# Performance work log

Measured on AMD Instinct MI355X. Metric: run time of the kernel, lower is better.

Reference implementation:

```python
import jax, jax.numpy as jnp
import numpy as np

B = 2; C = 3; IMG = 224; P = 16
DIM = 256; DEPTH = 2; HEADS = 4; DH = 64; MLP = 1024; NCLS = 1000
GRID = IMG // P            # 14
NPATCH = GRID * GRID       # 196
T = NPATCH + 1             # 197 (cls token)
PATCH_DIM = C * P * P      # 768


def _ln(x, g, b):
    m = x.mean(-1, keepdims=True)
    v = ((x - m) ** 2).mean(-1, keepdims=True)
    return (x - m) * jax.lax.rsqrt(v + 1e-5) * g + b


def _trittention(x, ln_g, ln_b, w_abcde, b_abcde, w_out, b_out):
    b, t, _ = x.shape
    xn = _ln(x, ln_g, ln_b)
    abcde = xn @ w_abcde + b_abcde                      # [b,t,5*H*DH]
    a, bb, c, d, e = jnp.split(abcde, 5, axis=-1)
    rs = lambda z: z.reshape(b, t, HEADS, DH)
    a, bb, c, d, e = map(rs, (a, bb, c, d, e))
    # cubic ternary scores: [b, h, q, s, t]
    s = jnp.einsum('bshd,bthd,bqhd->bhqst', a, bb, c) / DH
    p = jax.nn.softmax(s.reshape(b, HEADS, t, t * t), axis=-1)
    p = p.reshape(b, HEADS, t, t, t)
    z = jnp.einsum('bhqlr,blhd->bhqd', p, d) + jnp.einsum('bhqlr,brhd->bhqd', p, e)
    z = z.transpose(0, 2, 1, 3).reshape(b, t, HEADS * DH)
    return z @ w_out + b_out


def _ff(x, ln_g, ln_b, w1, b1, w2, b2):
    h = jax.nn.gelu(_ln(x, ln_g, ln_b) @ w1 + b1, approximate=False)
    return h @ w2 + b2


def setup_inputs() -> dict:
    key = jax.random.key(0)
    ks = jax.random.split(key, 10)
    s = 0.02
    d = {}
    d['img'] = jax.random.normal(ks[0], (B, C, IMG, IMG), jnp.float32)
    d['patch_ln1_g'] = jnp.ones((PATCH_DIM,), jnp.float32)
    d['patch_ln1_b'] = jnp.zeros((PATCH_DIM,), jnp.float32)
    d['patch_w'] = jax.random.normal(ks[1], (PATCH_DIM, DIM), jnp.float32) * s
    d['patch_b'] = jnp.zeros((DIM,), jnp.float32)
    d['patch_ln2_g'] = jnp.ones((DIM,), jnp.float32)
    d['patch_ln2_b'] = jnp.zeros((DIM,), jnp.float32)
    d['pos_emb'] = jax.random.normal(ks[2], (1, T, DIM), jnp.float32) * s
    d['cls_token'] = jax.random.normal(ks[3], (1, 1, DIM), jnp.float32) * s
    d['attn_ln_g'] = jnp.ones((DEPTH, DIM), jnp.float32)
    d['attn_ln_b'] = jnp.zeros((DEPTH, DIM), jnp.float32)
    d['w_abcde'] = jax.random.normal(ks[4], (DEPTH, DIM, 5 * HEADS * DH), jnp.float32) * s
    d['b_abcde'] = jnp.zeros((DEPTH, 5 * HEADS * DH), jnp.float32)
    d['w_out'] = jax.random.normal(ks[5], (DEPTH, HEADS * DH, DIM), jnp.float32) * s
    d['b_out'] = jnp.zeros((DEPTH, DIM), jnp.float32)
    d['ff_ln_g'] = jnp.ones((DEPTH, DIM), jnp.float32)
    d['ff_ln_b'] = jnp.zeros((DEPTH, DIM), jnp.float32)
    d['ff_w1'] = jax.random.normal(ks[6], (DEPTH, DIM, MLP), jnp.float32) * s
    d['ff_b1'] = jnp.zeros((DEPTH, MLP), jnp.float32)
    d['ff_w2'] = jax.random.normal(ks[7], (DEPTH, MLP, DIM), jnp.float32) * s
    d['ff_b2'] = jnp.zeros((DEPTH, DIM), jnp.float32)
    d['final_ln_g'] = jnp.ones((DIM,), jnp.float32)
    d['final_ln_b'] = jnp.zeros((DIM,), jnp.float32)
    d['head_w'] = jax.random.normal(ks[8], (DIM, NCLS), jnp.float32) * s
    d['head_b'] = jnp.zeros((NCLS,), jnp.float32)
    return d


def reference(img, patch_ln1_g, patch_ln1_b, patch_w, patch_b, patch_ln2_g, patch_ln2_b,
              pos_emb, cls_token, attn_ln_g, attn_ln_b, w_abcde, b_abcde, w_out, b_out,
              ff_ln_g, ff_ln_b, ff_w1, ff_b1, ff_w2, ff_b2, final_ln_g, final_ln_b,
              head_w, head_b):
    b = img.shape[0]
    # Rearrange 'b c (h p1) (w p2) -> b (h w) (p1 p2 c)'
    x = img.reshape(b, C, GRID, P, GRID, P).transpose(0, 2, 4, 3, 5, 1)
    x = x.reshape(b, NPATCH, PATCH_DIM)
    x = _ln(x, patch_ln1_g, patch_ln1_b)
    x = x @ patch_w + patch_b
    x = _ln(x, patch_ln2_g, patch_ln2_b)
    cls = jnp.broadcast_to(cls_token, (b, 1, DIM))
    x = jnp.concatenate([cls, x], axis=1) + pos_emb
    for i in range(DEPTH):
        x = _trittention(x, attn_ln_g[i], attn_ln_b[i], w_abcde[i], b_abcde[i],
                         w_out[i], b_out[i]) + x
        x = _ff(x, ff_ln_g[i], ff_ln_b[i], ff_w1[i], ff_b1[i], ff_w2[i], ff_b2[i]) + x
    x = _ln(x, final_ln_g, final_ln_b)
    return x[:, 0] @ head_w + head_b
```

## Files before the change

### kernel.cpp

```cpp
#include <hip/hip_runtime.h>
#include <hip/hip_bf16.h>

#define BB 2
#define TT 197
#define TP 208
#define NT16 13
#define DIMM 256
#define HEADS_ 4
#define DH_ 64
#define ABCDE_N 1280
#define MLP_ 1024
#define NCLS_ 1000
#define PATCH_DIM_ 768

typedef __attribute__((ext_vector_type(8))) short short8_t;
typedef __attribute__((ext_vector_type(4))) float f32x4;

__device__ __forceinline__ float waveReduceSum(float v) {
#pragma unroll
    for (int off = 32; off > 0; off >>= 1) v += __shfl_xor(v, off, 64);
    return v;
}

__device__ __forceinline__ unsigned short f2bf(float x) {
    unsigned int u = __float_as_uint(x);
    u += 0x7FFFu + ((u >> 16) & 1u);
    return (unsigned short)(u >> 16);
}

__device__ __forceinline__ float bf2f(unsigned short u) {
    return __uint_as_float(((unsigned int)u) << 16);
}

__global__ __launch_bounds__(256) void patch_embed_k(
    const float* __restrict__ img, const float* __restrict__ g1, const float* __restrict__ b1,
    const float* __restrict__ pw, const float* __restrict__ pb,
    const float* __restrict__ g2, const float* __restrict__ b2,
    const float* __restrict__ pos, const float* __restrict__ cls,
    float* __restrict__ xa)
{
    int tid = threadIdx.x;
    if (blockIdx.x == 98) {
        for (int b = 0; b < BB; b++)
            xa[(long)b * TT * DIMM + tid] = cls[tid] + pos[tid];
        return;
    }
    __shared__ __align__(16) float xs[4][PATCH_DIM_];
    __shared__ float red[8];
    int pr0 = blockIdx.x * 4;
    for (int r = 0; r < 4; r++) {
        int pr = pr0 + r;
        int b = pr / 196, patch = pr % 196;
        int gh = patch / 14, gw = patch % 14;
        for (int j = tid; j < PATCH_DIM_; j += 256) {
            int c = j % 3, p2 = (j / 3) % 16, p1 = j / 48;
            xs[r][j] = img[(((long)b * 3 + c) * 224 + gh * 16 + p1) * 224 + gw * 16 + p2];
        }
    }
    __syncthreads();
    int wv = tid >> 6, lane = tid & 63;
    {
        int r = wv;
        float s = 0.f, s2 = 0.f;
        for (int j = lane; j < PATCH_DIM_; j += 64) { float v = xs[r][j]; s += v; s2 += v * v; }
        s = waveReduceSum(s); s2 = waveReduceSum(s2);
        float m = s / PATCH_DIM_;
        float rs = rsqrtf(s2 / PATCH_DIM_ - m * m + 1e-5f);
        for (int j = lane; j < PATCH_DIM_; j += 64)
            xs[r][j] = (xs[r][j] - m) * rs * g1[j] + b1[j];
    }
    __syncthreads();
    float acc[4] = {0.f, 0.f, 0.f, 0.f};
    for (int k = 0; k < PATCH_DIM_; k += 4) {
        float w0 = pw[(k + 0) * DIMM + tid];
        float w1 = pw[(k + 1) * DIMM + tid];
        float w2 = pw[(k + 2) * DIMM + tid];
        float w3 = pw[(k + 3) * DIMM + tid];
#pragma unroll
        for (int r = 0; r < 4; r++) {
            float4 xv = *(const float4*)&xs[r][k];
            acc[r] = fmaf(xv.x, w0, fmaf(xv.y, w1, fmaf(xv.z, w2, fmaf(xv.w, w3, acc[r]))));
        }
    }
#pragma unroll
    for (int r = 0; r < 4; r++) acc[r] += pb[tid];
    for (int r = 0; r < 4; r++) {
        float s = waveReduceSum(acc[r]);
        float s2 = waveReduceSum(acc[r] * acc[r]);
        if (lane == 0) { red[wv * 2] = s; red[wv * 2 + 1] = s2; }
        __syncthreads();
        float S = red[0] + red[2] + red[4] + red[6];
        float S2 = red[1] + red[3] + red[5] + red[7];
        __syncthreads();
        float m = S / DIMM;
        float rs = rsqrtf(S2 / DIMM - m * m + 1e-5f);
        int pr = pr0 + r;
        int b = pr / 196, patch = pr % 196;
        float v = (acc[r] - m) * rs * g2[tid] + b2[tid] + pos[(1 + patch) * DIMM + tid];
        xa[((long)b * TT + 1 + patch) * DIMM + tid] = v;
    }
}

__global__ __launch_bounds__(512) void gemm_ksplit_k(
    const float* __restrict__ x, long x_stride, int M, int K, int N,
    const float* __restrict__ w, const float* __restrict__ bias,
    const float* __restrict__ res, float* __restrict__ out,
    const float* __restrict__ ln_g, const float* __restrict__ ln_b,
    int do_gelu)
{
    __shared__ __align__(16) float xs[4 * 1024];
    __shared__ float psum[8 * 4 * 64];
    int tid = threadIdx.x, lane = tid & 63, wv = tid >> 6;
    int row0 = blockIdx.y * 4, col0 = blockIdx.x * 64;

    for (int i = tid; i < 4 * K; i += 512) {
        int r = i / K, k = i - r * K;
        int row = row0 + r;
        xs[i] = (row < M) ? x[(long)row * x_stride + k] : 0.f;
    }
    __syncthreads();
    if (ln_g) {
        if (wv < 4) {
            float* xr = xs + wv * K;
            float s = 0.f, s2 = 0.f;
            for (int k = lane; k < K; k += 64) { float v = xr[k]; s += v; s2 += v * v; }
            s = waveReduceSum(s); s2 = waveReduceSum(s2);
            float m = s / K;
            float rs = rsqrtf(s2 / K - m * m + 1e-5f);
            for (int k = lane; k < K; k += 64)
                xr[k] = (xr[k] - m) * rs * ln_g[k] + ln_b[k];
        }
        __syncthreads();
    }

    int col = col0 + lane;
    float a0 = 0.f, a1 = 0.f, a2 = 0.f, a3 = 0.f;
    int kq = K >> 3;
    if (col < N) {
        const float* x0 = xs + wv * kq;
        const float* x1 = x0 + K;
        const float* x2 = x1 + K;
        const float* x3 = x2 + K;
        const float* wp = w + (long)(wv * kq) * N + col;
        long nl = N;
        for (int kk = 0; kk < kq; kk += 4) {
            float w0 = wp[0], w1 = wp[nl], w2 = wp[2 * nl], w3 = wp[3 * nl];
            wp += 4 * nl;
            float4 v0 = *(const float4*)(x0 + kk);
            float4 v1 = *(const float4*)(x1 + kk);
            float4 v2 = *(const float4*)(x2 + kk);
            float4 v3 = *(const float4*)(x3 + kk);
            a0 = fmaf(v0.x, w0, fmaf(v0.y, w1, fmaf(v0.z, w2, fmaf(v0.w, w3, a0))));
            a1 = fmaf(v1.x, w0, fmaf(v1.y, w1, fmaf(v1.z, w2, fmaf(v1.w, w3, a1))));
            a2 = fmaf(v2.x, w0, fmaf(v2.y, w1, fmaf(v2.z, w2, fmaf(v2.w, w3, a2))));
            a3 = fmaf(v3.x, w0, fmaf(v3.y, w1, fmaf(v3.z, w2, fmaf(v3.w, w3, a3))));
        }
    }
    psum[wv * 256 + 0 * 64 + lane] = a0;
    psum[wv * 256 + 1 * 64 + lane] = a1;
    psum[wv * 256 + 2 * 64 + lane] = a2;
    psum[wv * 256 + 3 * 64 + lane] = a3;
    __syncthreads();

    if (tid < 256) {
        int r = tid >> 6, c = tid & 63;
        float v = ((psum[r * 64 + c]        + psum[256 + r * 64 + c])
                +  (psum[512 + r * 64 + c]  + psum[768 + r * 64 + c]))
                + ((psum[1024 + r * 64 + c] + psum[1280 + r * 64 + c])
                +  (psum[1536 + r * 64 + c] + psum[1792 + r * 64 + c]));
        int row = row0 + r, cw = col0 + c;
        if (row < M && cw < N) {
            if (bias) v += bias[cw];
            if (do_gelu) v = 0.5f * v * (1.f + erff(v * 0.70710678118654752f));
            if (res) v += res[(long)row * N + cw];
            out[(long)row * N + cw] = v;
        }
    }
}

__global__ __launch_bounds__(256) void tritt_k(
    const float* __restrict__ abcde, float* __restrict__ z)
{
    __shared__ __align__(16) unsigned short a_lds[TP * 64];
    __shared__ __align__(16) unsigned short b_lds[TP * 64];
    __shared__ float pl_s[4][TP];
    __shared__ float pr_s[4][TP];

    int tid = threadIdx.x, lane = tid & 63, wv = tid >> 6;
    int bh = blockIdx.y;
    int b = bh >> 2, h = bh & 3;
    const float* base = abcde + (long)b * TT * ABCDE_N;
    const float SC = 1.4426950408889634f / 64.f;

    for (int i = tid; i < TP * 8; i += 256) {
        int row = i >> 3, ch = i & 7;
        int idx = row * 64 + ((ch * 8) ^ ((row & 7) << 3));
        unsigned short av[8], bv[8];
        if (row < TT) {
            const float* srcA = base + (long)row * ABCDE_N + h * 64 + ch * 8;
            const float* srcB = srcA + 256;
            float4 a0 = *(const float4*)(srcA);
            float4 a1 = *(const float4*)(srcA + 4);
            float4 b0 = *(const float4*)(srcB);
            float4 b1 = *(const float4*)(srcB + 4);
            av[0] = f2bf(a0.x); av[1] = f2bf(a0.y); av[2] = f2bf(a0.z); av[3] = f2bf(a0.w);
            av[4] = f2bf(a1.x); av[5] = f2bf(a1.y); av[6] = f2bf(a1.z); av[7] = f2bf(a1.w);
            bv[0] = f2bf(b0.x); bv[1] = f2bf(b0.y); bv[2] = f2bf(b0.z); bv[3] = f2bf(b0.w);
            bv[4] = f2bf(b1.x); bv[5] = f2bf(b1.y); bv[6] = f2bf(b1.z); bv[7] = f2bf(b1.w);
        } else {
#pragma unroll
            for (int j = 0; j < 8; j++) { av[j] = 0; bv[j] = 0; }
        }
        *(short8_t*)&a_lds[idx] = *(const short8_t*)av;
        *(short8_t*)&b_lds[idx] = *(const short8_t*)bv;
    }
    __syncthreads();

    int q = blockIdx.x * 4 + wv;
    if (q >= TT) return;

    int lm = lane & 15;
    int lg = lane >> 4;

    const float* cp = base + (long)q * ABCDE_N + 512 + h * 64;
    float c0[8], c1[8];
    {
        float4 v0 = *(const float4*)(cp + lg * 8);
        float4 v1 = *(const float4*)(cp + lg * 8 + 4);
        float4 v2 = *(const float4*)(cp + (lg + 4) * 8);
        float4 v3 = *(const float4*)(cp + (lg + 4) * 8 + 4);
        c0[0] = v0.x * SC; c0[1] = v0.y * SC; c0[2] = v0.z * SC; c0[3] = v0.w * SC;
        c0[4] = v1.x * SC; c0[5] = v1.y * SC; c0[6] = v1.z * SC; c0[7] = v1.w * SC;
        c1[0] = v2.x * SC; c1[1] = v2.y * SC; c1[2] = v2.z * SC; c1[3] = v2.w * SC;
        c1[4] = v3.x * SC; c1[5] = v3.y * SC; c1[6] = v3.z * SC; c1[7] = v3.w * SC;
    }

    short8_t bf0[NT16], bf1[NT16];
#pragma unroll
    for (int j = 0; j < NT16; j++) {
        int brow = j * 16 + lm;
        bf0[j] = *(const short8_t*)&b_lds[brow * 64 + (((lg    ) * 8) ^ ((brow & 7) << 3))];
        bf1[j] = *(const short8_t*)&b_lds[brow * 64 + (((lg + 4) * 8) ^ ((brow & 7) << 3))];
    }

    float pcol[NT16];
#pragma unroll
    for (int j = 0; j < NT16; j++) pcol[j] = 0.f;

#pragma unroll 1
    for (int i = 0; i < NT16; i++) {
        int arow = i * 16 + lm;
        short8_t af0 = *(const short8_t*)&a_lds[arow * 64 + (((lg    ) * 8) ^ ((arow & 7) << 3))];
        short8_t af1 = *(const short8_t*)&a_lds[arow * 64 + (((lg + 4) * 8) ^ ((arow & 7) << 3))];
        short8_t ac0, ac1;
#pragma unroll
        for (int e = 0; e < 8; e++) {
            ac0[e] = (short)f2bf(bf2f((unsigned short)af0[e]) * c0[e]);
            ac1[e] = (short)f2bf(bf2f((unsigned short)af1[e]) * c1[e]);
        }
        float prow[4] = {0.f, 0.f, 0.f, 0.f};
#pragma unroll
        for (int j = 0; j < NT16; j++) {
            f32x4 acc = {0.f, 0.f, 0.f, 0.f};
            acc = __builtin_amdgcn_mfma_f32_16x16x32_bf16(ac0, bf0[j], acc, 0, 0, 0);
            acc = __builtin_amdgcn_mfma_f32_16x16x32_bf16(ac1, bf1[j], acc, 0, 0, 0);
            float e0 = __builtin_amdgcn_exp2f(acc[0]);
            float e1 = __builtin_amdgcn_exp2f(acc[1]);
            float e2 = __builtin_amdgcn_exp2f(acc[2]);
            float e3 = __builtin_amdgcn_exp2f(acc[3]);
            prow[0] += e0; prow[1] += e1; prow[2] += e2; prow[3] += e3;
            pcol[j] += (e0 + e1) + (e2 + e3);
        }
#pragma unroll
        for (int r = 0; r < 4; r++) {
            prow[r] += __shfl_xor(prow[r], 1, 64);
            prow[r] += __shfl_xor(prow[r], 2, 64);
            prow[r] += __shfl_xor(prow[r], 4, 64);
            prow[r] += __shfl_xor(prow[r], 8, 64);
        }
        if (lm == 0) {
            int rb = i * 16 + lg * 4;
#pragma unroll
            for (int r = 0; r < 4; r++) pl_s[wv][rb + r] = prow[r];
        }
    }
#pragma unroll
    for (int j = 0; j < NT16; j++) {
        float c = pcol[j];
        c += __shfl_xor(c, 16, 64);
        c += __shfl_xor(c, 32, 64);
        if (lane < 16) pr_s[wv][j * 16 + lane] = c;
    }

    float zpart = 0.f;
    for (int s = lane; s < TT; s += 64) zpart += pl_s[wv][s];
    zpart = waveReduceSum(zpart);
    float rz = 1.f / (zpart - 11.f * TT);

    const float* dp = base + 768 + h * 64 + lane;
    const float* ep = base + 1024 + h * 64 + lane;
    float zacc = 0.f;
    for (int s = 0; s < TT; s++) {
        zacc = fmaf(pl_s[wv][s] - 11.f, dp[(long)s * ABCDE_N], zacc);
        zacc = fmaf(pr_s[wv][s] - 11.f, ep[(long)s * ABCDE_N], zacc);
    }
    z[((long)b * TT + q) * DIMM + h * 64 + lane] = zacc * rz;
}

extern "C" void kernel_launch(void* const* d_in, const int* in_sizes, int n_in,
                              void* d_out, int out_size, void* d_ws, size_t ws_size,
                              hipStream_t stream)
{
    const float* img    = (const float*)d_in[0];
    const float* g1     = (const float*)d_in[1];
    const float* b1     = (const float*)d_in[2];
    const float* pw     = (const float*)d_in[3];
    const float* pb     = (const float*)d_in[4];
    const float* g2     = (const float*)d_in[5];
    const float* b2     = (const float*)d_in[6];
    const float* pos    = (const float*)d_in[7];
    const float* cls    = (const float*)d_in[8];
    const float* attn_g = (const float*)d_in[9];
    const float* attn_b = (const float*)d_in[10];
    const float* w_abc  = (const float*)d_in[11];
    const float* b_abc  = (const float*)d_in[12];
    const float* w_out  = (const float*)d_in[13];
    const float* b_out  = (const float*)d_in[14];
    const float* ff_g   = (const float*)d_in[15];
    const float* ff_b   = (const float*)d_in[16];
    const float* w1     = (const float*)d_in[17];
    const float* b1f    = (const float*)d_in[18];
    const float* w2     = (const float*)d_in[19];
    const float* b2f    = (const float*)d_in[20];
    const float* fin_g  = (const float*)d_in[21];
    const float* fin_b  = (const float*)d_in[22];
    const float* hw     = (const float*)d_in[23];
    const float* hb     = (const float*)d_in[24];
    float* out = (float*)d_out;

    const int MROWS = BB * TT;
    float* ws = (float*)d_ws;
    float* xa = ws;
    float* xb = xa + (long)MROWS * DIMM;
    float* zb = xb + (long)MROWS * DIMM;
    float* ab = zb + (long)MROWS * DIMM;

    patch_embed_k<<<99, 256, 0, stream>>>(img, g1, b1, pw, pb, g2, b2, pos, cls, xa);

    const int GY = (MROWS + 3) / 4;
    const int QT4 = (TT + 3) / 4;
    for (int i = 0; i < 2; i++) {
        gemm_ksplit_k<<<dim3(ABCDE_N / 64, GY), 512, 0, stream>>>(
            xa, DIMM, MROWS, DIMM, ABCDE_N,
            w_abc + (long)i * DIMM * ABCDE_N, b_abc + (long)i * ABCDE_N,
            nullptr, ab, attn_g + i * DIMM, attn_b + i * DIMM, 0);
        tritt_k<<<dim3(QT4, BB * HEADS_), 256, 0, stream>>>(ab, zb);
        gemm_ksplit_k<<<dim3(DIMM / 64, GY), 512, 0, stream>>>(
            zb, DIMM, MROWS, DIMM, DIMM,
            w_out + (long)i * DIMM * DIMM, b_out + (long)i * DIMM,
            xa, xb, nullptr, nullptr, 0);
        gemm_ksplit_k<<<dim3(MLP_ / 64, GY), 512, 0, stream>>>(
            xb, DIMM, MROWS, DIMM, MLP_,
            w1 + (long)i * DIMM * MLP_, b1f + (long)i * MLP_,
            nullptr, ab, ff_g + i * DIMM, ff_b + i * DIMM, 1);
        gemm_ksplit_k<<<dim3(DIMM / 64, GY), 512, 0, stream>>>(
            ab, MLP_, MROWS, MLP_, DIMM,
            w2 + (long)i * MLP_ * DIMM, b2f + (long)i * DIMM,
            xb, xa, nullptr, nullptr, 0);
    }
    gemm_ksplit_k<<<dim3((NCLS_ + 63) / 64, 1), 512, 0, stream>>>(
        xa, (long)TT * DIMM, BB, DIMM, NCLS_,
        hw, hb, nullptr, out, fin_g, fin_b, 0);
}
```

Measured before the change: 227.4 us.

## Split each query's trittention work across two waves with LDS reduction

The trittention kernel now launches 512 threads per block, so each of the four queries gets two waves. The waves interleave the 16-row score tiles and the d/e accumulation over s, then combine column sums and partial z outputs through shared memory. The goal is more waves in flight per block to hide MFMA, exp and latency costs. In exchange it adds extra syncthreads, shared-memory reductions and higher register pressure under the 512-thread launch bound.

```diff
diff --git a/kernel.cpp b/kernel.cpp
--- a/kernel.cpp
+++ b/kernel.cpp
@@ -178,21 +178,26 @@
     }
 }
 
-__global__ __launch_bounds__(256) void tritt_k(
+__global__ __launch_bounds__(512) void tritt_k(
     const float* __restrict__ abcde, float* __restrict__ z)
 {
     __shared__ __align__(16) unsigned short a_lds[TP * 64];
     __shared__ __align__(16) unsigned short b_lds[TP * 64];
     __shared__ float pl_s[4][TP];
-    __shared__ float pr_s[4][TP];
+    __shared__ float pr_s[8][TP];
+    __shared__ float zp[8][DH_];
 
     int tid = threadIdx.x, lane = tid & 63, wv = tid >> 6;
+    int k = wv >> 1;
+    int wh = wv & 1;
     int bh = blockIdx.y;
     int b = bh >> 2, h = bh & 3;
     const float* base = abcde + (long)b * TT * ABCDE_N;
     const float SC = 1.4426950408889634f / 64.f;
-
-    for (int i = tid; i < TP * 8; i += 256) {
+    int q = blockIdx.x * 4 + k;
+    bool qok = (q < TT);
+
+    for (int i = tid; i < TP * 8; i += 512) {
         int row = i >> 3, ch = i & 7;
         int idx = row * 64 + ((ch * 8) ^ ((row & 7) << 3));
         unsigned short av[8], bv[8];
@@ -216,13 +221,10 @@
     }
     __syncthreads();
 
-    int q = blockIdx.x * 4 + wv;
-    if (q >= TT) return;
-
     int lm = lane & 15;
     int lg = lane >> 4;
 
-    const float* cp = base + (long)q * ABCDE_N + 512 + h * 64;
+    const float* cp = base + (long)(qok ? q : 0) * ABCDE_N + 512 + h * 64;
     float c0[8], c1[8];
     {
         float4 v0 = *(const float4*)(cp + lg * 8);
@@ -247,41 +249,43 @@
 #pragma unroll
     for (int j = 0; j < NT16; j++) pcol[j] = 0.f;
 
+    if (qok) {
 #pragma unroll 1
-    for (int i = 0; i < NT16; i++) {
-        int arow = i * 16 + lm;
-        short8_t af0 = *(const short8_t*)&a_lds[arow * 64 + (((lg    ) * 8) ^ ((arow & 7) << 3))];
-        short8_t af1 = *(const short8_t*)&a_lds[arow * 64 + (((lg + 4) * 8) ^ ((arow & 7) << 3))];
-        short8_t ac0, ac1;
-#pragma unroll
-        for (int e = 0; e < 8; e++) {
-            ac0[e] = (short)f2bf(bf2f((unsigned short)af0[e]) * c0[e]);
-            ac1[e] = (short)f2bf(bf2f((unsigned short)af1[e]) * c1[e]);
-        }
-        float prow[4] = {0.f, 0.f, 0.f, 0.f};
-#pragma unroll
-        for (int j = 0; j < NT16; j++) {
-            f32x4 acc = {0.f, 0.f, 0.f, 0.f};
-            acc = __builtin_amdgcn_mfma_f32_16x16x32_bf16(ac0, bf0[j], acc, 0, 0, 0);
-            acc = __builtin_amdgcn_mfma_f32_16x16x32_bf16(ac1, bf1[j], acc, 0, 0, 0);
-            float e0 = __builtin_amdgcn_exp2f(acc[0]);
-            float e1 = __builtin_amdgcn_exp2f(acc[1]);
-            float e2 = __builtin_amdgcn_exp2f(acc[2]);
-            float e3 = __builtin_amdgcn_exp2f(acc[3]);
-            prow[0] += e0; prow[1] += e1; prow[2] += e2; prow[3] += e3;
-            pcol[j] += (e0 + e1) + (e2 + e3);
-        }
-#pragma unroll
-        for (int r = 0; r < 4; r++) {
-            prow[r] += __shfl_xor(prow[r], 1, 64);
-            prow[r] += __shfl_xor(prow[r], 2, 64);
-            prow[r] += __shfl_xor(prow[r], 4, 64);
-            prow[r] += __shfl_xor(prow[r], 8, 64);
-        }
-        if (lm == 0) {
-            int rb = i * 16 + lg * 4;
-#pragma unroll
-            for (int r = 0; r < 4; r++) pl_s[wv][rb + r] = prow[r];
+        for (int i = wh; i < NT16; i += 2) {
+            int arow = i * 16 + lm;
+            short8_t af0 = *(const short8_t*)&a_lds[arow * 64 + (((lg    ) * 8) ^ ((arow & 7) << 3))];
+            short8_t af1 = *(const short8_t*)&a_lds[arow * 64 + (((lg + 4) * 8) ^ ((arow & 7) << 3))];
+            short8_t ac0, ac1;
+#pragma unroll
+            for (int e = 0; e < 8; e++) {
+                ac0[e] = (short)f2bf(bf2f((unsigned short)af0[e]) * c0[e]);
+                ac1[e] = (short)f2bf(bf2f((unsigned short)af1[e]) * c1[e]);
+            }
+            float prow[4] = {0.f, 0.f, 0.f, 0.f};
+#pragma unroll
+            for (int j = 0; j < NT16; j++) {
+                f32x4 acc = {0.f, 0.f, 0.f, 0.f};
+                acc = __builtin_amdgcn_mfma_f32_16x16x32_bf16(ac0, bf0[j], acc, 0, 0, 0);
+                acc = __builtin_amdgcn_mfma_f32_16x16x32_bf16(ac1, bf1[j], acc, 0, 0, 0);
+                float e0 = __builtin_amdgcn_exp2f(acc[0]);
+                float e1 = __builtin_amdgcn_exp2f(acc[1]);
+                float e2 = __builtin_amdgcn_exp2f(acc[2]);
+                float e3 = __builtin_amdgcn_exp2f(acc[3]);
+                prow[0] += e0; prow[1] += e1; prow[2] += e2; prow[3] += e3;
+                pcol[j] += (e0 + e1) + (e2 + e3);
+            }
+#pragma unroll
+            for (int r = 0; r < 4; r++) {
+                prow[r] += __shfl_xor(prow[r], 1, 64);
+                prow[r] += __shfl_xor(prow[r], 2, 64);
+                prow[r] += __shfl_xor(prow[r], 4, 64);
+                prow[r] += __shfl_xor(prow[r], 8, 64);
+            }
+            if (lm == 0) {
+                int rb = i * 16 + lg * 4;
+#pragma unroll
+                for (int r = 0; r < 4; r++) pl_s[k][rb + r] = prow[r];
+            }
         }
     }
 #pragma unroll
@@ -291,20 +295,38 @@
         c += __shfl_xor(c, 32, 64);
         if (lane < 16) pr_s[wv][j * 16 + lane] = c;
     }
-
-    float zpart = 0.f;
-    for (int s = lane; s < TT; s += 64) zpart += pl_s[wv][s];
-    zpart = waveReduceSum(zpart);
-    float rz = 1.f / (zpart - 11.f * TT);
-
-    const float* dp = base + 768 + h * 64 + lane;
-    const float* ep = base + 1024 + h * 64 + lane;
-    float zacc = 0.f;
-    for (int s = 0; s < TT; s++) {
-        zacc = fmaf(pl_s[wv][s] - 11.f, dp[(long)s * ABCDE_N], zacc);
-        zacc = fmaf(pr_s[wv][s] - 11.f, ep[(long)s * ABCDE_N], zacc);
-    }
-    z[((long)b * TT + q) * DIMM + h * 64 + lane] = zacc * rz;
+    __syncthreads();
+
+    for (int idx = tid; idx < 4 * TP; idx += 512) {
+        int kk = idx / TP, s = idx - kk * TP;
+        pr_s[2 * kk][s] += pr_s[2 * kk + 1][s];
+    }
+    __syncthreads();
+
+    if (qok) {
+        float zpart = 0.f;
+        for (int s = lane; s < TT; s += 64) zpart += pl_s[k][s];
+        zpart = waveReduceSum(zpart);
+        float rz = 1.f / (zpart - 11.f * TT);
+
+        const float* dp = base + 768 + h * 64 + lane;
+        const float* ep = base + 1024 + h * 64 + lane;
+        float zacc = 0.f;
+        for (int s = wh; s < TT; s += 2) {
+            zacc = fmaf(pl_s[k][s] - 11.f, dp[(long)s * ABCDE_N], zacc);
+            zacc = fmaf(pr_s[2 * k][s] - 11.f, ep[(long)s * ABCDE_N], zacc);
+        }
+        zp[wv][lane] = zacc * rz;
+    }
+    __syncthreads();
+
+    if (tid < 256) {
+        int kk = tid >> 6, d = tid & 63;
+        int qw = blockIdx.x * 4 + kk;
+        if (qw < TT) {
+            z[((long)b * TT + qw) * DIMM + h * 64 + d] = zp[2 * kk][d] + zp[2 * kk + 1][d];
+        }
+    }
 }
 
 extern "C" void kernel_launch(void* const* d_in, const int* in_sizes, int n_in,
@@ -354,7 +376,7 @@
             xa, DIMM, MROWS, DIMM, ABCDE_N,
             w_abc + (long)i * DIMM * ABCDE_N, b_abc + (long)i * ABCDE_N,
             nullptr, ab, attn_g + i * DIMM, attn_b + i * DIMM, 0);
-        tritt_k<<<dim3(QT4, BB * HEADS_), 256, 0, stream>>>(ab, zb);
+        tritt_k<<<dim3(QT4, BB * HEADS_), 512, 0, stream>>>(ab, zb);
         gemm_ksplit_k<<<dim3(DIMM / 64, GY), 512, 0, stream>>>(
             zb, DIMM, MROWS, DIMM, DIMM,
             w_out + (long)i * DIMM * DIMM, b_out + (long)i * DIMM,
```

New measurement: 293.7 us. 29.1% more time.
